# Optimization experiments

Measured on AMD Instinct MI355X. Metric: run time of the kernel, lower is better.

## Reference

```python
import jax, jax.numpy as jnp
import numpy as np


def mha(x, mask, wq, bq, wk, bk, wv, bv, wo, bo, n_heads):
    # Flaubert/XLM MultiHeadAttention (eval mode, dropout = identity).
    bs, qlen, dim = x.shape
    dph = dim // n_heads

    def split_heads(t):  # (bs, qlen, dim) -> (bs, n_heads, qlen, dph)
        return t.reshape(bs, qlen, n_heads, dph).transpose(0, 2, 1, 3)

    q = split_heads(x @ wq + bq) / jnp.sqrt(jnp.asarray(dph, x.dtype))
    k = split_heads(x @ wk + bk)
    v = split_heads(x @ wv + bv)

    scores = jnp.einsum('bhqd,bhkd->bhqk', q, k)  # (bs, h, qlen, klen)
    neg = jnp.finfo(scores.dtype).min
    scores = jnp.where((mask == 0)[:, None, None, :], neg, scores)
    weights = jax.nn.softmax(scores, axis=-1)
    ctx = jnp.einsum('bhqk,bhkd->bhqd', weights, v)
    ctx = ctx.transpose(0, 2, 1, 3).reshape(bs, qlen, dim)
    return ctx @ wo + bo


def setup_inputs() -> dict:
    key = jax.random.key(0)
    ks = jax.random.split(key, 20)
    bs, slen = 4, 1024
    d0, d1 = 192, 66
    std = 0.02
    inp = {
        'x': jax.random.normal(ks[0], (bs, slen, d0), jnp.float32),
        'y': jax.random.normal(ks[1], (bs, slen, d1), jnp.float32),
        'mask0': jax.random.randint(ks[2], (bs, slen), 0, 2, jnp.int32),
        'mask1': jax.random.randint(ks[3], (bs, slen), 0, 2, jnp.int32),
    }
    names0 = ['q0', 'k0', 'v0', 'o0']
    names1 = ['q1', 'k1', 'v1', 'o1']
    for i, n in enumerate(names0):
        inp[n + '_w'] = jax.random.normal(ks[4 + i], (d0, d0), jnp.float32) * std
        inp[n + '_b'] = jnp.zeros((d0,), jnp.float32)
    for i, n in enumerate(names1):
        inp[n + '_w'] = jax.random.normal(ks[8 + i], (d1, d1), jnp.float32) * std
        inp[n + '_b'] = jnp.zeros((d1,), jnp.float32)
    return inp


def reference(x, y, mask0, mask1,
              q0_w, q0_b, k0_w, k0_b, v0_w, v0_b, o0_w, o0_b,
              q1_w, q1_b, k1_w, k1_b, v1_w, v1_b, o1_w, o1_b):
    out0 = mha(x, mask0, q0_w, q0_b, k0_w, k0_b, v0_w, v0_b, o0_w, o0_b, n_heads=16)
    out1 = mha(y, mask1, q1_w, q1_b, k1_w, k1_b, v1_w, v1_b, o1_w, o1_b, n_heads=11)
    return (out0, out1)
```

## Files before the change

### kernel.cpp

```cpp
#include <hip/hip_runtime.h>
#include <math.h>


#define BS 4
#define SLEN 1024

#define Q0_OFF 0
#define C0_OFF 786432
#define Q1_OFF 1572864
#define C1_OFF 1843200
#define K0H_OFF 2113536
#define V0T_OFF 2506752
#define K1H_OFF 2899968
#define V1T_OFF 3080192
#define CNT_OFF 3223552

#define OUT0_SIZE 786432

#if __has_builtin(__builtin_amdgcn_exp2f)
#define EXP2(x) __builtin_amdgcn_exp2f(x)
#else
#define EXP2(x) __expf((x) * 0.69314718056f)
#endif

typedef _Float16 f16x2 __attribute__((ext_vector_type(2)));
typedef _Float16 f16x4 __attribute__((ext_vector_type(4)));
typedef _Float16 f16x8 __attribute__((ext_vector_type(8)));
typedef float f32x4 __attribute__((ext_vector_type(4)));

__device__ __forceinline__ void mfma_chunk(const _Float16* sA, const _Float16* sWT,
                                           int wv, int lane, f32x4 acc[4])
{
  const int col = lane & 15, grp = lane >> 4;
#pragma unroll
  for (int ks = 0; ks < 2; ++ks) {
    const f16x8 bf = *(const f16x8*)(sWT + (wv * 16 + col) * 72 + ks * 32 + grp * 8);
#pragma unroll
    for (int mt = 0; mt < 4; ++mt) {
      const f16x8 af = *(const f16x8*)(sA + (mt * 16 + col) * 72 + ks * 32 + grp * 8);
      acc[mt] = __builtin_amdgcn_mfma_f32_16x16x32_f16(af, bf, acc[mt], 0, 0, 0);
    }
  }
}

__device__ __forceinline__ void mfma_chunk_split(
    const _Float16* sAh, const _Float16* sAl,
    const _Float16* sWTh, const _Float16* sWTl,
    int wv, int lane, f32x4 acc[4])
{
  const int col = lane & 15, grp = lane >> 4;
#pragma unroll
  for (int ks = 0; ks < 2; ++ks) {
    const int boff = (wv * 16 + col) * 72 + ks * 32 + grp * 8;
    const f16x8 bh = *(const f16x8*)(sWTh + boff);
    const f16x8 bl = *(const f16x8*)(sWTl + boff);
#pragma unroll
    for (int mt = 0; mt < 4; ++mt) {
      const int aoff = (mt * 16 + col) * 72 + ks * 32 + grp * 8;
      const f16x8 ah = *(const f16x8*)(sAh + aoff);
      const f16x8 al = *(const f16x8*)(sAl + aoff);
      acc[mt] = __builtin_amdgcn_mfma_f32_16x16x32_f16(ah, bh, acc[mt], 0, 0, 0);
      acc[mt] = __builtin_amdgcn_mfma_f32_16x16x32_f16(ah, bl, acc[mt], 0, 0, 0);
      acc[mt] = __builtin_amdgcn_mfma_f32_16x16x32_f16(al, bh, acc[mt], 0, 0, 0);
    }
  }
}

template <int DIM, int H, int DPH, int NT, int NCH, int KST>
__device__ void qkv_impl(int bid, const float* __restrict__ X,
                         const int* __restrict__ mask,
                         const float* __restrict__ qw, const float* __restrict__ qb,
                         const float* __restrict__ kw, const float* __restrict__ kb,
                         const float* __restrict__ vw, const float* __restrict__ vb,
                         float* __restrict__ qo, _Float16* __restrict__ kh,
                         _Float16* __restrict__ vth, int* __restrict__ cnt_out,
                         char* smem)
{
  const int mt64 = bid & 63;
  const int rest = bid >> 6;
  const int mat = rest / NT;
  const int nt = rest % NT;
  const int row0 = mt64 * 64, col0 = nt * 64;

  const float* W = (mat == 0) ? qw : (mat == 1) ? kw : vw;
  const float* B = (mat == 0) ? qb : (mat == 1) ? kb : vb;
  const float scale = (mat == 0) ? (1.44269504089f / sqrtf((float)DPH)) : 1.0f;

  _Float16* sA = (_Float16*)smem;
  _Float16* sWT = sA + 64 * 72;
  int* sSP = (int*)(smem + 2 * 64 * 72 * 2);

  const int tid = threadIdx.x;
  const int wv = tid >> 6, lane = tid & 63;

  float2 rA[8], rW[8];
  auto qprefetch = [&](int c) {
    const int kc = c * 64;
#pragma unroll
    for (int t = 0; t < 8; ++t) {
      const int idx = tid + t * 256;
      {
        const int m = idx >> 5, k = (idx & 31) * 2;
        rA[t] = (kc + k < DIM)
                    ? *(const float2*)(X + (size_t)(row0 + m) * DIM + kc + k)
                    : make_float2(0.f, 0.f);
      }
      {
        const int k = idx >> 5, n = (idx & 31) * 2;
        rW[t] = (kc + k < DIM && col0 + n < DIM)
                    ? *(const float2*)(W + (size_t)(kc + k) * DIM + col0 + n)
                    : make_float2(0.f, 0.f);
      }
    }
  };
  auto qcommit = [&]() {
#pragma unroll
    for (int t = 0; t < 8; ++t) {
      const int idx = tid + t * 256;
      {
        const int m = idx >> 5, k = (idx & 31) * 2;
        *(f16x2*)(sA + m * 72 + k) = (f16x2){(_Float16)rA[t].x, (_Float16)rA[t].y};
      }
      {
        const int k = idx >> 5, n = (idx & 31) * 2;
        sWT[n * 72 + k] = (_Float16)rW[t].x;
        sWT[(n + 1) * 72 + k] = (_Float16)rW[t].y;
      }
    }
  };

  qprefetch(0);

  if (mat != 0) {
    int* sS = (int*)smem;
    const int b = row0 >> 10;
    const int* m = mask + (b << 10);
    int mv[4], s4 = 0;
#pragma unroll
    for (int i = 0; i < 4; ++i) { mv[i] = m[tid * 4 + i] ? 1 : 0; s4 += mv[i]; }
    sS[tid] = s4;
    __syncthreads();
    for (int off = 1; off < 256; off <<= 1) {
      const int v = sS[tid];
      const int add = (tid >= off) ? sS[tid - off] : 0;
      __syncthreads();
      sS[tid] = v + add;
      __syncthreads();
    }
    const int tot = sS[255];
    int u = tid ? sS[tid - 1] : 0;
    const int s0 = row0 & 1023;
#pragma unroll
    for (int i = 0; i < 4; ++i) {
      const int s = tid * 4 + i;
      const int sp = mv[i] ? u : tot + (s - u);
      u += mv[i];
      const unsigned rel = (unsigned)(s - s0);
      if (rel < 64u) sSP[rel] = sp;
    }
    if (mat == 1 && nt == 0 && s0 == 0 && tid == 0) cnt_out[b] = tot;
    __syncthreads();
  }

  f32x4 acc[4] = {{0.f,0.f,0.f,0.f},{0.f,0.f,0.f,0.f},{0.f,0.f,0.f,0.f},{0.f,0.f,0.f,0.f}};

  for (int c = 0; c < NCH; ++c) {
    __syncthreads();
    qcommit();
    __syncthreads();
    if (c + 1 < NCH) qprefetch(c + 1);
    mfma_chunk(sA, sWT, wv, lane, acc);
  }

  const int col = lane & 15, grp = lane >> 4;
  const int cidx = col0 + wv * 16 + col;
  if (cidx < DIM) {
    const float bias = B[cidx];
    const int h = cidx / DPH, d = cidx % DPH;
#pragma unroll
    for (int mt = 0; mt < 4; ++mt) {
#pragma unroll
      for (int r = 0; r < 4; ++r) {
        const int m = row0 + mt * 16 + grp * 4 + r;
        const int b = m >> 10, s = m & 1023;
        const float v = acc[mt][r] + bias;
        const int bh = b * H + h;
        if (mat == 0) {
          qo[(size_t)((bh << 10) + s) * DPH + d] = v * scale;
        } else {
          const int sp = sSP[mt * 16 + grp * 4 + r];
          if (mat == 1)
            kh[(size_t)((bh << 10) + sp) * KST + d] = (_Float16)v;
          else
            vth[((size_t)(bh * DPH + d) << 10) + sp] = (_Float16)v;
        }
      }
    }
  }
}

__global__ __launch_bounds__(256) void qkv_kernel(
    const float* __restrict__ x, const float* __restrict__ y,
    const int* __restrict__ mask0, const int* __restrict__ mask1,
    const float* __restrict__ q0w, const float* __restrict__ q0b,
    const float* __restrict__ k0w, const float* __restrict__ k0b,
    const float* __restrict__ v0w, const float* __restrict__ v0b,
    const float* __restrict__ q1w, const float* __restrict__ q1b,
    const float* __restrict__ k1w, const float* __restrict__ k1b,
    const float* __restrict__ v1w, const float* __restrict__ v1b,
    float* __restrict__ ws)
{
  extern __shared__ char smem[];
  _Float16* hws = (_Float16*)ws;
  int* cnts = (int*)(ws + CNT_OFF);
  const int bid = blockIdx.x;
  if (bid < 576)
    qkv_impl<192, 16, 12, 3, 3, 12>(bid, x, mask0, q0w, q0b, k0w, k0b, v0w, v0b,
                                    ws + Q0_OFF, hws + 2 * (size_t)K0H_OFF,
                                    hws + 2 * (size_t)V0T_OFF, cnts, smem);
  else
    qkv_impl<66, 11, 6, 2, 2, 8>(bid - 576, y, mask1, q1w, q1b, k1w, k1b, v1w, v1b,
                                 ws + Q1_OFF, hws + 2 * (size_t)K1H_OFF,
                                 hws + 2 * (size_t)V1T_OFF, cnts + 4, smem);
}

template <int H, int DPH, int SKP>
__device__ void attn_impl(int bid, const float* __restrict__ qg,
                          const _Float16* __restrict__ kh,
                          const _Float16* __restrict__ vth,
                          const int* __restrict__ cnts,
                          float* __restrict__ ctx, char* smem)
{
  constexpr int CH = 128;
  constexpr int KBUF = CH * SKP + 32;
  constexpr int VST = 136;

  _Float16* sK = (_Float16*)smem;
  _Float16* sVT = sK + 2 * KBUF;

  const int bh = bid >> 4;
  const int b = bh / H;
  const int h = bh % H;
  const int tid = threadIdx.x;

  const float* qb_ = qg + (size_t)bh * SLEN * DPH;
  const _Float16* kb_ = kh + (size_t)bh * SLEN * SKP;
  const _Float16* vb_ = vth + ((size_t)bh * DPH << 10);
  const int cnt = cnts[b];
  const int nch = (cnt + CH - 1) >> 7;

  if (tid < 64) sK[(tid >> 5) * KBUF + CH * SKP + (tid & 31)] = (_Float16)0.f;

  const int wave = tid >> 6, lane = tid & 63;
  const int col = lane & 15, grp = lane >> 4;
  const int qtile = (bid & 15) * 4 + wave;

  f16x4 aq;
  {
    const int qrow = qtile * 16 + col;
#pragma unroll
    for (int j = 0; j < 4; ++j) {
      const int d = grp * 4 + j;
      aq[j] = (d < DPH) ? (_Float16)qb_[(size_t)qrow * DPH + d] : (_Float16)0.f;
    }
  }

  constexpr int kN = CH * SKP / 8;
  constexpr int vN = DPH * 16;
  const int vd = tid >> 4, vq = tid & 15;
  uint4 pk, pv;
  auto prefetch = [&](int cc) {
    if (tid < kN) pk = ((const uint4*)(kb_ + (size_t)cc * CH * SKP))[tid];
    if (tid < vN) pv = ((const uint4*)(vb_ + ((size_t)vd << 10) + cc * CH))[vq];
  };
  auto commit = [&](int pb) {
    if (tid < kN) ((uint4*)(sK + pb * KBUF))[tid] = pk;
    if (tid < vN) *(uint4*)(sVT + (pb * DPH + vd) * VST + vq * 8) = pv;
  };

  prefetch(0);
  commit(0);
  __syncthreads();

  f32x4 Oacc[2] = {{0.f,0.f,0.f,0.f},{0.f,0.f,0.f,0.f}};
  float lsum = 0.f;
  const int de = (col < DPH) ? col : 0;

#pragma unroll 1
  for (int c = 0; c < nch; ++c) {
    const int p = c & 1;
    if (c + 1 < nch) prefetch(c + 1);

    const _Float16* sKp = sK + p * KBUF;
    const _Float16* sVp = sVT + p * DPH * VST;
    const int keyr = c * CH + grp * 4;

#pragma unroll
    for (int kt = 0; kt < CH / 16; ++kt) {
      const f16x4 kf = *(const f16x4*)(sKp + (kt * 16 + col) * SKP + grp * 4);
      const int k0 = keyr + kt * 16;
      const f32x4 biasv = {(k0 < cnt) ? 0.f : -100.f,
                           (k0 + 1 < cnt) ? 0.f : -100.f,
                           (k0 + 2 < cnt) ? 0.f : -100.f,
                           (k0 + 3 < cnt) ? 0.f : -100.f};
      const f32x4 S = __builtin_amdgcn_mfma_f32_16x16x16f16(kf, aq, biasv,
                                                            0, 0, 0);
      const float e0 = EXP2(S[0]), e1 = EXP2(S[1]);
      const float e2 = EXP2(S[2]), e3 = EXP2(S[3]);
      lsum += (e0 + e1) + (e2 + e3);
      const f16x4 pf = {(_Float16)e0, (_Float16)e1, (_Float16)e2, (_Float16)e3};
      const f16x4 vf = *(const f16x4*)(sVp + de * VST + kt * 16 + grp * 4);
      Oacc[kt & 1] = __builtin_amdgcn_mfma_f32_16x16x16f16(pf, vf, Oacc[kt & 1],
                                                           0, 0, 0);
    }

    if (c + 1 < nch) commit(p ^ 1);
    __syncthreads();
  }

  f32x4 Osum;
#pragma unroll
  for (int r = 0; r < 4; ++r) Osum[r] = Oacc[0][r] + Oacc[1][r];
  float lred = lsum;
  lred += __shfl_xor(lred, 16);
  lred += __shfl_xor(lred, 32);
  float lq[4];
#pragma unroll
  for (int r = 0; r < 4; ++r) lq[r] = __shfl(lred, grp * 4 + r);
  if (col < DPH) {
    const int qrow0 = qtile * 16;
#pragma unroll
    for (int r = 0; r < 4; ++r) {
      const int row = qrow0 + grp * 4 + r;
      ctx[(size_t)(b * SLEN + row) * (H * DPH) + h * DPH + col] = Osum[r] / lq[r];
    }
  }
}

__global__ __launch_bounds__(256) void attn_kernel(float* __restrict__ ws)
{
  extern __shared__ char smem[];
  _Float16* hws = (_Float16*)ws;
  const int* cnts = (const int*)(ws + CNT_OFF);
  const int bid = blockIdx.x;
  if (bid < 1024)
    attn_impl<16, 12, 12>(bid, ws + Q0_OFF, hws + 2 * (size_t)K0H_OFF,
                          hws + 2 * (size_t)V0T_OFF, cnts, ws + C0_OFF, smem);
  else
    attn_impl<11, 6, 8>(bid - 1024, ws + Q1_OFF, hws + 2 * (size_t)K1H_OFF,
                        hws + 2 * (size_t)V1T_OFF, cnts + 4, ws + C1_OFF, smem);
}

template <int DIM, int NCH>
__device__ void oproj_impl(int bid, const float* __restrict__ Cx,
                           const float* __restrict__ ow, const float* __restrict__ ob,
                           float* __restrict__ out, char* smem)
{
  const int mt64 = bid & 63;
  const int nt = bid >> 6;
  const int row0 = mt64 * 64, col0 = nt * 64;

  _Float16* sAh = (_Float16*)smem;
  _Float16* sAl = sAh + 64 * 72;
  _Float16* sWTh = sAl + 64 * 72;
  _Float16* sWTl = sWTh + 64 * 72;

  const int tid = threadIdx.x;
  const int wv = tid >> 6, lane = tid & 63;

  float2 rA[8], rW[8];
  auto oprefetch = [&](int c) {
    const int kc = c * 64;
#pragma unroll
    for (int t = 0; t < 8; ++t) {
      const int idx = tid + t * 256;
      {
        const int m = idx >> 5, k = (idx & 31) * 2;
        rA[t] = (kc + k < DIM)
                    ? *(const float2*)(Cx + (size_t)(row0 + m) * DIM + kc + k)
                    : make_float2(0.f, 0.f);
      }
      {
        const int k = idx >> 5, n = (idx & 31) * 2;
        rW[t] = (kc + k < DIM && col0 + n < DIM)
                    ? *(const float2*)(ow + (size_t)(kc + k) * DIM + col0 + n)
                    : make_float2(0.f, 0.f);
      }
    }
  };
  auto ocommit = [&]() {
#pragma unroll
    for (int t = 0; t < 8; ++t) {
      const int idx = tid + t * 256;
      {
        const int m = idx >> 5, k = (idx & 31) * 2;
        const _Float16 hx = (_Float16)rA[t].x, hy = (_Float16)rA[t].y;
        *(f16x2*)(sAh + m * 72 + k) = (f16x2){hx, hy};
        *(f16x2*)(sAl + m * 72 + k) =
            (f16x2){(_Float16)(rA[t].x - (float)hx), (_Float16)(rA[t].y - (float)hy)};
      }
      {
        const int k = idx >> 5, n = (idx & 31) * 2;
        const _Float16 hx = (_Float16)rW[t].x, hy = (_Float16)rW[t].y;
        sWTh[n * 72 + k] = hx;
        sWTh[(n + 1) * 72 + k] = hy;
        sWTl[n * 72 + k] = (_Float16)(rW[t].x - (float)hx);
        sWTl[(n + 1) * 72 + k] = (_Float16)(rW[t].y - (float)hy);
      }
    }
  };

  oprefetch(0);

  f32x4 acc[4] = {{0.f,0.f,0.f,0.f},{0.f,0.f,0.f,0.f},{0.f,0.f,0.f,0.f},{0.f,0.f,0.f,0.f}};

  for (int c = 0; c < NCH; ++c) {
    __syncthreads();
    ocommit();
    __syncthreads();
    if (c + 1 < NCH) oprefetch(c + 1);
    mfma_chunk_split(sAh, sAl, sWTh, sWTl, wv, lane, acc);
  }

  const int col = lane & 15, grp = lane >> 4;
  const int cidx = col0 + wv * 16 + col;
  if (cidx < DIM) {
    const float bias = ob[cidx];
#pragma unroll
    for (int mt = 0; mt < 4; ++mt) {
#pragma unroll
      for (int r = 0; r < 4; ++r) {
        const int m = row0 + mt * 16 + grp * 4 + r;
        out[(size_t)m * DIM + cidx] = acc[mt][r] + bias;
      }
    }
  }
}

__global__ __launch_bounds__(256) void oproj_kernel(
    const float* __restrict__ o0w, const float* __restrict__ o0b,
    const float* __restrict__ o1w, const float* __restrict__ o1b,
    float* __restrict__ ws, float* __restrict__ out)
{
  extern __shared__ char smem[];
  const int bid = blockIdx.x;
  if (bid < 192)
    oproj_impl<192, 3>(bid, ws + C0_OFF, o0w, o0b, out, smem);
  else
    oproj_impl<66, 2>(bid - 192, ws + C1_OFF, o1w, o1b, out + OUT0_SIZE, smem);
}

extern "C" void kernel_launch(void* const* d_in, const int* in_sizes, int n_in,
                              void* d_out, int out_size, void* d_ws, size_t ws_size,
                              hipStream_t stream)
{
  const float* x = (const float*)d_in[0];
  const float* y = (const float*)d_in[1];
  const int* mask0 = (const int*)d_in[2];
  const int* mask1 = (const int*)d_in[3];
  const float* q0w = (const float*)d_in[4];  const float* q0b = (const float*)d_in[5];
  const float* k0w = (const float*)d_in[6];  const float* k0b = (const float*)d_in[7];
  const float* v0w = (const float*)d_in[8];  const float* v0b = (const float*)d_in[9];
  const float* o0w = (const float*)d_in[10]; const float* o0b = (const float*)d_in[11];
  const float* q1w = (const float*)d_in[12]; const float* q1b = (const float*)d_in[13];
  const float* k1w = (const float*)d_in[14]; const float* k1b = (const float*)d_in[15];
  const float* v1w = (const float*)d_in[16]; const float* v1b = (const float*)d_in[17];
  const float* o1w = (const float*)d_in[18]; const float* o1b = (const float*)d_in[19];

  float* ws = (float*)d_ws;
  float* out = (float*)d_out;

  const int qkv_smem = 2 * 64 * 72 * 2 + 64 * 4;
  const int oproj_smem = 4 * 64 * 72 * 2;
  const int attn_smem = 2 * (128 * 12 + 32) * 2 + 2 * 12 * 136 * 2;

  qkv_kernel<<<960, 256, qkv_smem, stream>>>(x, y, mask0, mask1,
                                             q0w, q0b, k0w, k0b, v0w, v0b,
                                             q1w, q1b, k1w, k1b, v1w, v1b, ws);
  attn_kernel<<<1728, 256, attn_smem, stream>>>(ws);
  oproj_kernel<<<320, 256, oproj_smem, stream>>>(o0w, o0b, o1w, o1b, ws, out);
}
```

Before: 144.4 us.

## Fuse output projection into attention via last-head-done atomic counter

```diff
diff --git a/kernel.cpp b/kernel.cpp
--- a/kernel.cpp
+++ b/kernel.cpp
@@ -14,6 +14,11 @@
 #define K1H_OFF 2899968
 #define V1T_OFF 3080192
 #define CNT_OFF 3223552
+#define GRP_OFF 3223560
+#define WT0H_OFF 3223696
+#define WT0L_OFF 3242128
+#define WT1H_OFF 3260560
+#define WT1L_OFF 3263728
 
 #define OUT0_SIZE 786432
 
@@ -39,29 +44,6 @@
     for (int mt = 0; mt < 4; ++mt) {
       const f16x8 af = *(const f16x8*)(sA + (mt * 16 + col) * 72 + ks * 32 + grp * 8);
       acc[mt] = __builtin_amdgcn_mfma_f32_16x16x32_f16(af, bf, acc[mt], 0, 0, 0);
-    }
-  }
-}
-
-__device__ __forceinline__ void mfma_chunk_split(
-    const _Float16* sAh, const _Float16* sAl,
-    const _Float16* sWTh, const _Float16* sWTl,
-    int wv, int lane, f32x4 acc[4])
-{
-  const int col = lane & 15, grp = lane >> 4;
-#pragma unroll
-  for (int ks = 0; ks < 2; ++ks) {
-    const int boff = (wv * 16 + col) * 72 + ks * 32 + grp * 8;
-    const f16x8 bh = *(const f16x8*)(sWTh + boff);
-    const f16x8 bl = *(const f16x8*)(sWTl + boff);
-#pragma unroll
-    for (int mt = 0; mt < 4; ++mt) {
-      const int aoff = (mt * 16 + col) * 72 + ks * 32 + grp * 8;
-      const f16x8 ah = *(const f16x8*)(sAh + aoff);
-      const f16x8 al = *(const f16x8*)(sAl + aoff);
-      acc[mt] = __builtin_amdgcn_mfma_f32_16x16x32_f16(ah, bh, acc[mt], 0, 0, 0);
-      acc[mt] = __builtin_amdgcn_mfma_f32_16x16x32_f16(ah, bl, acc[mt], 0, 0, 0);
-      acc[mt] = __builtin_amdgcn_mfma_f32_16x16x32_f16(al, bh, acc[mt], 0, 0, 0);
     }
   }
 }
@@ -199,6 +181,34 @@
   }
 }
 
+__device__ void qkv_aux(int aid, const float* __restrict__ o0w,
+                        const float* __restrict__ o1w,
+                        _Float16* __restrict__ wt0h, _Float16* __restrict__ wt0l,
+                        _Float16* __restrict__ wt1h, _Float16* __restrict__ wt1l,
+                        int* __restrict__ grp)
+{
+  const int tid = threadIdx.x;
+  if (aid == 0 && tid < 128) grp[tid] = 0;
+  if (aid < 6) {
+    for (int e = aid * 6144 + tid; e < (aid + 1) * 6144; e += 256) {
+      const int n = e / 192, k = e - n * 192;
+      const float v = o0w[k * 192 + n];
+      const _Float16 h = (_Float16)v;
+      wt0h[n * 192 + k] = h;
+      wt0l[n * 192 + k] = (_Float16)(v - (float)h);
+    }
+  } else {
+    const int a = aid - 6;
+    for (int e = a * 3168 + tid; e < (a + 1) * 3168; e += 256) {
+      const int n = e / 96, k = e - n * 96;
+      const float v = (k < 66) ? o1w[k * 66 + n] : 0.f;
+      const _Float16 h = (_Float16)v;
+      wt1h[n * 96 + k] = h;
+      wt1l[n * 96 + k] = (_Float16)(v - (float)h);
+    }
+  }
+}
+
 __global__ __launch_bounds__(256) void qkv_kernel(
     const float* __restrict__ x, const float* __restrict__ y,
     const int* __restrict__ mask0, const int* __restrict__ mask1,
@@ -208,12 +218,20 @@
     const float* __restrict__ q1w, const float* __restrict__ q1b,
     const float* __restrict__ k1w, const float* __restrict__ k1b,
     const float* __restrict__ v1w, const float* __restrict__ v1b,
+    const float* __restrict__ o0w, const float* __restrict__ o1w,
     float* __restrict__ ws)
 {
   extern __shared__ char smem[];
   _Float16* hws = (_Float16*)ws;
   int* cnts = (int*)(ws + CNT_OFF);
   const int bid = blockIdx.x;
+  if (bid >= 960) {
+    qkv_aux(bid - 960, o0w, o1w,
+            hws + 2 * (size_t)WT0H_OFF, hws + 2 * (size_t)WT0L_OFF,
+            hws + 2 * (size_t)WT1H_OFF, hws + 2 * (size_t)WT1L_OFF,
+            (int*)(ws + GRP_OFF));
+    return;
+  }
   if (bid < 576)
     qkv_impl<192, 16, 12, 3, 3, 12>(bid, x, mask0, q0w, q0b, k0w, k0b, v0w, v0b,
                                     ws + Q0_OFF, hws + 2 * (size_t)K0H_OFF,
@@ -224,12 +242,17 @@
                                  hws + 2 * (size_t)V1T_OFF, cnts + 4, smem);
 }
 
-template <int H, int DPH, int SKP>
+template <int H, int DPH, int SKP, int DIMo, int NT, int NKB, int KP, bool VEC>
 __device__ void attn_impl(int bid, const float* __restrict__ qg,
                           const _Float16* __restrict__ kh,
                           const _Float16* __restrict__ vth,
                           const int* __restrict__ cnts,
-                          float* __restrict__ ctx, char* smem)
+                          float* __restrict__ ctx,
+                          const _Float16* __restrict__ WTh,
+                          const _Float16* __restrict__ WTl,
+                          const float* __restrict__ obias,
+                          float* __restrict__ outp,
+                          int* __restrict__ grp, int gbase, char* smem)
 {
   constexpr int CH = 128;
   constexpr int KBUF = CH * SKP + 32;
@@ -252,7 +275,7 @@
   if (tid < 64) sK[(tid >> 5) * KBUF + CH * SKP + (tid & 31)] = (_Float16)0.f;
 
   const int wave = tid >> 6, lane = tid & 63;
-  const int col = lane & 15, grp = lane >> 4;
+  const int col = lane & 15, grpq = lane >> 4;
   const int qtile = (bid & 15) * 4 + wave;
 
   f16x4 aq;
@@ -260,7 +283,7 @@
     const int qrow = qtile * 16 + col;
 #pragma unroll
     for (int j = 0; j < 4; ++j) {
-      const int d = grp * 4 + j;
+      const int d = grpq * 4 + j;
       aq[j] = (d < DPH) ? (_Float16)qb_[(size_t)qrow * DPH + d] : (_Float16)0.f;
     }
   }
@@ -293,11 +316,11 @@
 
     const _Float16* sKp = sK + p * KBUF;
     const _Float16* sVp = sVT + p * DPH * VST;
-    const int keyr = c * CH + grp * 4;
+    const int keyr = c * CH + grpq * 4;
 
 #pragma unroll
     for (int kt = 0; kt < CH / 16; ++kt) {
-      const f16x4 kf = *(const f16x4*)(sKp + (kt * 16 + col) * SKP + grp * 4);
+      const f16x4 kf = *(const f16x4*)(sKp + (kt * 16 + col) * SKP + grpq * 4);
       const int k0 = keyr + kt * 16;
       const f32x4 biasv = {(k0 < cnt) ? 0.f : -100.f,
                            (k0 + 1 < cnt) ? 0.f : -100.f,
@@ -309,7 +332,7 @@
       const float e2 = EXP2(S[2]), e3 = EXP2(S[3]);
       lsum += (e0 + e1) + (e2 + e3);
       const f16x4 pf = {(_Float16)e0, (_Float16)e1, (_Float16)e2, (_Float16)e3};
-      const f16x4 vf = *(const f16x4*)(sVp + de * VST + kt * 16 + grp * 4);
+      const f16x4 vf = *(const f16x4*)(sVp + de * VST + kt * 16 + grpq * 4);
       Oacc[kt & 1] = __builtin_amdgcn_mfma_f32_16x16x16f16(pf, vf, Oacc[kt & 1],
                                                            0, 0, 0);
     }
@@ -326,128 +349,104 @@
   lred += __shfl_xor(lred, 32);
   float lq[4];
 #pragma unroll
-  for (int r = 0; r < 4; ++r) lq[r] = __shfl(lred, grp * 4 + r);
+  for (int r = 0; r < 4; ++r) lq[r] = __shfl(lred, grpq * 4 + r);
   if (col < DPH) {
     const int qrow0 = qtile * 16;
 #pragma unroll
     for (int r = 0; r < 4; ++r) {
-      const int row = qrow0 + grp * 4 + r;
+      const int row = qrow0 + grpq * 4 + r;
       ctx[(size_t)(b * SLEN + row) * (H * DPH) + h * DPH + col] = Osum[r] / lq[r];
     }
   }
-}
-
-__global__ __launch_bounds__(256) void attn_kernel(float* __restrict__ ws)
+
+  __threadfence();
+  __syncthreads();
+  int* flag = (int*)smem;
+  if (tid == 0) {
+    const int g = gbase + b * 16 + (bid & 15);
+    flag[0] = (atomicAdd(&grp[g], 1) == H - 1) ? 1 : 0;
+  }
+  __syncthreads();
+  if (!flag[0]) return;
+  __threadfence();
+
+  const int strip = bid & 15;
+  const float* Crow = ctx + (size_t)(b * SLEN + strip * 64) * DIMo;
+  float* Orow = outp + (size_t)(b * SLEN + strip * 64) * DIMo;
+
+#pragma unroll 1
+  for (int nt = 0; nt < NT; ++nt) {
+    const int cidx = nt * 64 + wave * 16 + col;
+    f32x4 oacc[4] = {{0.f,0.f,0.f,0.f},{0.f,0.f,0.f,0.f},
+                     {0.f,0.f,0.f,0.f},{0.f,0.f,0.f,0.f}};
+#pragma unroll
+    for (int kb = 0; kb < NKB; ++kb) {
+      const int k0 = kb * 32 + grpq * 8;
+      f16x8 bhf = {}, blf = {};
+      if (cidx < DIMo) {
+        bhf = *(const f16x8*)(WTh + (size_t)cidx * KP + k0);
+        blf = *(const f16x8*)(WTl + (size_t)cidx * KP + k0);
+      }
+#pragma unroll
+      for (int mt = 0; mt < 4; ++mt) {
+        const int row_a = mt * 16 + col;
+        f16x8 ah, al;
+        if (VEC) {
+          const float* ap = Crow + (size_t)row_a * DIMo + k0;
+          const f32x4 v0 = *(const f32x4*)(ap);
+          const f32x4 v1 = *(const f32x4*)(ap + 4);
+#pragma unroll
+          for (int j = 0; j < 4; ++j) {
+            const _Float16 h0 = (_Float16)v0[j];
+            ah[j] = h0; al[j] = (_Float16)(v0[j] - (float)h0);
+            const _Float16 h1 = (_Float16)v1[j];
+            ah[4 + j] = h1; al[4 + j] = (_Float16)(v1[j] - (float)h1);
+          }
+        } else {
+#pragma unroll
+          for (int j = 0; j < 8; ++j) {
+            const int k = k0 + j;
+            const float v = (k < DIMo) ? Crow[(size_t)row_a * DIMo + k] : 0.f;
+            const _Float16 hh = (_Float16)v;
+            ah[j] = hh; al[j] = (_Float16)(v - (float)hh);
+          }
+        }
+        oacc[mt] = __builtin_amdgcn_mfma_f32_16x16x32_f16(ah, bhf, oacc[mt], 0, 0, 0);
+        oacc[mt] = __builtin_amdgcn_mfma_f32_16x16x32_f16(ah, blf, oacc[mt], 0, 0, 0);
+        oacc[mt] = __builtin_amdgcn_mfma_f32_16x16x32_f16(al, bhf, oacc[mt], 0, 0, 0);
+      }
+    }
+    if (cidx < DIMo) {
+      const float bias = obias[cidx];
+#pragma unroll
+      for (int mt = 0; mt < 4; ++mt)
+#pragma unroll
+        for (int r = 0; r < 4; ++r)
+          Orow[(size_t)(mt * 16 + grpq * 4 + r) * DIMo + cidx] = oacc[mt][r] + bias;
+    }
+  }
+}
+
+__global__ __launch_bounds__(256) void attn_kernel(
+    float* __restrict__ ws, float* __restrict__ out,
+    const float* __restrict__ o0b, const float* __restrict__ o1b)
 {
   extern __shared__ char smem[];
   _Float16* hws = (_Float16*)ws;
   const int* cnts = (const int*)(ws + CNT_OFF);
+  int* grp = (int*)(ws + GRP_OFF);
   const int bid = blockIdx.x;
   if (bid < 1024)
-    attn_impl<16, 12, 12>(bid, ws + Q0_OFF, hws + 2 * (size_t)K0H_OFF,
-                          hws + 2 * (size_t)V0T_OFF, cnts, ws + C0_OFF, smem);
+    attn_impl<16, 12, 12, 192, 3, 6, 192, true>(
+        bid, ws + Q0_OFF, hws + 2 * (size_t)K0H_OFF, hws + 2 * (size_t)V0T_OFF,
+        cnts, ws + C0_OFF, hws + 2 * (size_t)WT0H_OFF, hws + 2 * (size_t)WT0L_OFF,
+        o0b, out, grp, 0, smem);
   else
-    attn_impl<11, 6, 8>(bid - 1024, ws + Q1_OFF, hws + 2 * (size_t)K1H_OFF,
-                        hws + 2 * (size_t)V1T_OFF, cnts + 4, ws + C1_OFF, smem);
-}
-
-template <int DIM, int NCH>
-__device__ void oproj_impl(int bid, const float* __restrict__ Cx,
-                           const float* __restrict__ ow, const float* __restrict__ ob,
-                           float* __restrict__ out, char* smem)
-{
-  const int mt64 = bid & 63;
-  const int nt = bid >> 6;
-  const int row0 = mt64 * 64, col0 = nt * 64;
-
-  _Float16* sAh = (_Float16*)smem;
-  _Float16* sAl = sAh + 64 * 72;
-  _Float16* sWTh = sAl + 64 * 72;
-  _Float16* sWTl = sWTh + 64 * 72;
-
-  const int tid = threadIdx.x;
-  const int wv = tid >> 6, lane = tid & 63;
-
-  float2 rA[8], rW[8];
-  auto oprefetch = [&](int c) {
-    const int kc = c * 64;
-#pragma unroll
-    for (int t = 0; t < 8; ++t) {
-      const int idx = tid + t * 256;
-      {
-        const int m = idx >> 5, k = (idx & 31) * 2;
-        rA[t] = (kc + k < DIM)
-                    ? *(const float2*)(Cx + (size_t)(row0 + m) * DIM + kc + k)
-                    : make_float2(0.f, 0.f);
-      }
-      {
-        const int k = idx >> 5, n = (idx & 31) * 2;
-        rW[t] = (kc + k < DIM && col0 + n < DIM)
-                    ? *(const float2*)(ow + (size_t)(kc + k) * DIM + col0 + n)
-                    : make_float2(0.f, 0.f);
-      }
-    }
-  };
-  auto ocommit = [&]() {
-#pragma unroll
-    for (int t = 0; t < 8; ++t) {
-      const int idx = tid + t * 256;
-      {
-        const int m = idx >> 5, k = (idx & 31) * 2;
-        const _Float16 hx = (_Float16)rA[t].x, hy = (_Float16)rA[t].y;
-        *(f16x2*)(sAh + m * 72 + k) = (f16x2){hx, hy};
-        *(f16x2*)(sAl + m * 72 + k) =
-            (f16x2){(_Float16)(rA[t].x - (float)hx), (_Float16)(rA[t].y - (float)hy)};
-      }
-      {
-        const int k = idx >> 5, n = (idx & 31) * 2;
-        const _Float16 hx = (_Float16)rW[t].x, hy = (_Float16)rW[t].y;
-        sWTh[n * 72 + k] = hx;
-        sWTh[(n + 1) * 72 + k] = hy;
-        sWTl[n * 72 + k] = (_Float16)(rW[t].x - (float)hx);
-        sWTl[(n + 1) * 72 + k] = (_Float16)(rW[t].y - (float)hy);
-      }
-    }
-  };
-
-  oprefetch(0);
-
-  f32x4 acc[4] = {{0.f,0.f,0.f,0.f},{0.f,0.f,0.f,0.f},{0.f,0.f,0.f,0.f},{0.f,0.f,0.f,0.f}};
-
-  for (int c = 0; c < NCH; ++c) {
-    __syncthreads();
-    ocommit();
-    __syncthreads();
-    if (c + 1 < NCH) oprefetch(c + 1);
-    mfma_chunk_split(sAh, sAl, sWTh, sWTl, wv, lane, acc);
-  }
-
-  const int col = lane & 15, grp = lane >> 4;
-  const int cidx = col0 + wv * 16 + col;
-  if (cidx < DIM) {
-    const float bias = ob[cidx];
-#pragma unroll
-    for (int mt = 0; mt < 4; ++mt) {
-#pragma unroll
-      for (int r = 0; r < 4; ++r) {
-        const int m = row0 + mt * 16 + grp * 4 + r;
-        out[(size_t)m * DIM + cidx] = acc[mt][r] + bias;
-      }
-    }
-  }
-}
-
-__global__ __launch_bounds__(256) void oproj_kernel(
-    const float* __restrict__ o0w, const float* __restrict__ o0b,
-    const float* __restrict__ o1w, const float* __restrict__ o1b,
-    float* __restrict__ ws, float* __restrict__ out)
-{
-  extern __shared__ char smem[];
-  const int bid = blockIdx.x;
-  if (bid < 192)
-    oproj_impl<192, 3>(bid, ws + C0_OFF, o0w, o0b, out, smem);
-  else
-    oproj_impl<66, 2>(bid - 192, ws + C1_OFF, o1w, o1b, out + OUT0_SIZE, smem);
+    attn_impl<11, 6, 8, 66, 2, 3, 96, false>(
+        bid - 1024, ws + Q1_OFF, hws + 2 * (size_t)K1H_OFF,
+        hws + 2 * (size_t)V1T_OFF, cnts + 4, ws + C1_OFF,
+        hws + 2 * (size_t)WT1H_OFF, hws + 2 * (size_t)WT1L_OFF,
+        o1b, out + OUT0_SIZE, grp, 64, smem);
 }
 
 extern "C" void kernel_launch(void* const* d_in, const int* in_sizes, int n_in,
@@ -471,12 +470,11 @@
   float* out = (float*)d_out;
 
   const int qkv_smem = 2 * 64 * 72 * 2 + 64 * 4;
-  const int oproj_smem = 4 * 64 * 72 * 2;
   const int attn_smem = 2 * (128 * 12 + 32) * 2 + 2 * 12 * 136 * 2;
 
-  qkv_kernel<<<960, 256, qkv_smem, stream>>>(x, y, mask0, mask1,
+  qkv_kernel<<<968, 256, qkv_smem, stream>>>(x, y, mask0, mask1,
                                              q0w, q0b, k0w, k0b, v0w, v0b,
-                                             q1w, q1b, k1w, k1b, v1w, v1b, ws);
-  attn_kernel<<<1728, 256, attn_smem, stream>>>(ws);
-  oproj_kernel<<<320, 256, oproj_smem, stream>>>(o0w, o0b, o1w, o1b, ws, out);
-}
+                                             q1w, q1b, k1w, k1b, v1w, v1b,
+                                             o0w, o1w, ws);
+  attn_kernel<<<1728, 256, attn_smem, stream>>>(ws, out, o0b, o1b);
+}
```

Result: slower. 323.2 us (+123.7%).

## Process two query tiles per wave in attention and halve oproj row tiles

Applied to the files above, without the earlier changes.

```diff
diff --git a/kernel.cpp b/kernel.cpp
--- a/kernel.cpp
+++ b/kernel.cpp
@@ -43,10 +43,11 @@
   }
 }
 
+template <int MT>
 __device__ __forceinline__ void mfma_chunk_split(
     const _Float16* sAh, const _Float16* sAl,
     const _Float16* sWTh, const _Float16* sWTl,
-    int wv, int lane, f32x4 acc[4])
+    int wv, int lane, f32x4 acc[MT])
 {
   const int col = lane & 15, grp = lane >> 4;
 #pragma unroll
@@ -55,7 +56,7 @@
     const f16x8 bh = *(const f16x8*)(sWTh + boff);
     const f16x8 bl = *(const f16x8*)(sWTl + boff);
 #pragma unroll
-    for (int mt = 0; mt < 4; ++mt) {
+    for (int mt = 0; mt < MT; ++mt) {
       const int aoff = (mt * 16 + col) * 72 + ks * 32 + grp * 8;
       const f16x8 ah = *(const f16x8*)(sAh + aoff);
       const f16x8 al = *(const f16x8*)(sAl + aoff);
@@ -238,7 +239,7 @@
   _Float16* sK = (_Float16*)smem;
   _Float16* sVT = sK + 2 * KBUF;
 
-  const int bh = bid >> 4;
+  const int bh = bid >> 3;
   const int b = bh / H;
   const int h = bh % H;
   const int tid = threadIdx.x;
@@ -253,15 +254,17 @@
 
   const int wave = tid >> 6, lane = tid & 63;
   const int col = lane & 15, grp = lane >> 4;
-  const int qtile = (bid & 15) * 4 + wave;
-
-  f16x4 aq;
-  {
-    const int qrow = qtile * 16 + col;
+  const int strip = bid & 7;
+  const int qt[2] = {strip * 8 + wave, strip * 8 + 4 + wave};
+
+  f16x4 aq[2];
+#pragma unroll
+  for (int i = 0; i < 2; ++i) {
+    const int qrow = qt[i] * 16 + col;
 #pragma unroll
     for (int j = 0; j < 4; ++j) {
       const int d = grp * 4 + j;
-      aq[j] = (d < DPH) ? (_Float16)qb_[(size_t)qrow * DPH + d] : (_Float16)0.f;
+      aq[i][j] = (d < DPH) ? (_Float16)qb_[(size_t)qrow * DPH + d] : (_Float16)0.f;
     }
   }
 
@@ -282,8 +285,9 @@
   commit(0);
   __syncthreads();
 
-  f32x4 Oacc[2] = {{0.f,0.f,0.f,0.f},{0.f,0.f,0.f,0.f}};
-  float lsum = 0.f;
+  f32x4 Oacc[2][2] = {{{0.f,0.f,0.f,0.f},{0.f,0.f,0.f,0.f}},
+                      {{0.f,0.f,0.f,0.f},{0.f,0.f,0.f,0.f}}};
+  float lsum[2] = {0.f, 0.f};
   const int de = (col < DPH) ? col : 0;
 
 #pragma unroll 1
@@ -303,36 +307,49 @@
                            (k0 + 1 < cnt) ? 0.f : -100.f,
                            (k0 + 2 < cnt) ? 0.f : -100.f,
                            (k0 + 3 < cnt) ? 0.f : -100.f};
-      const f32x4 S = __builtin_amdgcn_mfma_f32_16x16x16f16(kf, aq, biasv,
-                                                            0, 0, 0);
-      const float e0 = EXP2(S[0]), e1 = EXP2(S[1]);
-      const float e2 = EXP2(S[2]), e3 = EXP2(S[3]);
-      lsum += (e0 + e1) + (e2 + e3);
-      const f16x4 pf = {(_Float16)e0, (_Float16)e1, (_Float16)e2, (_Float16)e3};
+      const f32x4 S0 = __builtin_amdgcn_mfma_f32_16x16x16f16(kf, aq[0], biasv,
+                                                             0, 0, 0);
+      const f32x4 S1 = __builtin_amdgcn_mfma_f32_16x16x16f16(kf, aq[1], biasv,
+                                                             0, 0, 0);
       const f16x4 vf = *(const f16x4*)(sVp + de * VST + kt * 16 + grp * 4);
-      Oacc[kt & 1] = __builtin_amdgcn_mfma_f32_16x16x16f16(pf, vf, Oacc[kt & 1],
-                                                           0, 0, 0);
+      const float a0 = EXP2(S0[0]), a1 = EXP2(S0[1]);
+      const float a2 = EXP2(S0[2]), a3 = EXP2(S0[3]);
+      lsum[0] += (a0 + a1) + (a2 + a3);
+      const f16x4 pf0 = {(_Float16)a0, (_Float16)a1, (_Float16)a2, (_Float16)a3};
+      Oacc[0][kt & 1] = __builtin_amdgcn_mfma_f32_16x16x16f16(pf0, vf,
+                                                              Oacc[0][kt & 1],
+                                                              0, 0, 0);
+      const float b0 = EXP2(S1[0]), b1 = EXP2(S1[1]);
+      const float b2 = EXP2(S1[2]), b3 = EXP2(S1[3]);
+      lsum[1] += (b0 + b1) + (b2 + b3);
+      const f16x4 pf1 = {(_Float16)b0, (_Float16)b1, (_Float16)b2, (_Float16)b3};
+      Oacc[1][kt & 1] = __builtin_amdgcn_mfma_f32_16x16x16f16(pf1, vf,
+                                                              Oacc[1][kt & 1],
+                                                              0, 0, 0);
     }
 
     if (c + 1 < nch) commit(p ^ 1);
     __syncthreads();
   }
 
-  f32x4 Osum;
-#pragma unroll
-  for (int r = 0; r < 4; ++r) Osum[r] = Oacc[0][r] + Oacc[1][r];
-  float lred = lsum;
-  lred += __shfl_xor(lred, 16);
-  lred += __shfl_xor(lred, 32);
-  float lq[4];
-#pragma unroll
-  for (int r = 0; r < 4; ++r) lq[r] = __shfl(lred, grp * 4 + r);
-  if (col < DPH) {
-    const int qrow0 = qtile * 16;
-#pragma unroll
-    for (int r = 0; r < 4; ++r) {
-      const int row = qrow0 + grp * 4 + r;
-      ctx[(size_t)(b * SLEN + row) * (H * DPH) + h * DPH + col] = Osum[r] / lq[r];
+#pragma unroll
+  for (int i = 0; i < 2; ++i) {
+    f32x4 Osum;
+#pragma unroll
+    for (int r = 0; r < 4; ++r) Osum[r] = Oacc[i][0][r] + Oacc[i][1][r];
+    float lred = lsum[i];
+    lred += __shfl_xor(lred, 16);
+    lred += __shfl_xor(lred, 32);
+    float lq[4];
+#pragma unroll
+    for (int r = 0; r < 4; ++r) lq[r] = __shfl(lred, grp * 4 + r);
+    if (col < DPH) {
+      const int qrow0 = qt[i] * 16;
+#pragma unroll
+      for (int r = 0; r < 4; ++r) {
+        const int row = qrow0 + grp * 4 + r;
+        ctx[(size_t)(b * SLEN + row) * (H * DPH) + h * DPH + col] = Osum[r] / lq[r];
+      }
     }
   }
 }
@@ -343,11 +360,11 @@
   _Float16* hws = (_Float16*)ws;
   const int* cnts = (const int*)(ws + CNT_OFF);
   const int bid = blockIdx.x;
-  if (bid < 1024)
+  if (bid < 512)
     attn_impl<16, 12, 12>(bid, ws + Q0_OFF, hws + 2 * (size_t)K0H_OFF,
                           hws + 2 * (size_t)V0T_OFF, cnts, ws + C0_OFF, smem);
   else
-    attn_impl<11, 6, 8>(bid - 1024, ws + Q1_OFF, hws + 2 * (size_t)K1H_OFF,
+    attn_impl<11, 6, 8>(bid - 512, ws + Q1_OFF, hws + 2 * (size_t)K1H_OFF,
                         hws + 2 * (size_t)V1T_OFF, cnts + 4, ws + C1_OFF, smem);
 }
 
@@ -356,70 +373,70 @@
                            const float* __restrict__ ow, const float* __restrict__ ob,
                            float* __restrict__ out, char* smem)
 {
-  const int mt64 = bid & 63;
-  const int nt = bid >> 6;
-  const int row0 = mt64 * 64, col0 = nt * 64;
+  const int mt128 = bid & 127;
+  const int nt = bid >> 7;
+  const int row0 = mt128 * 32, col0 = nt * 64;
 
   _Float16* sAh = (_Float16*)smem;
-  _Float16* sAl = sAh + 64 * 72;
-  _Float16* sWTh = sAl + 64 * 72;
+  _Float16* sAl = sAh + 32 * 72;
+  _Float16* sWTh = sAl + 32 * 72;
   _Float16* sWTl = sWTh + 64 * 72;
 
   const int tid = threadIdx.x;
   const int wv = tid >> 6, lane = tid & 63;
 
-  float2 rA[8], rW[8];
+  float2 rA[4], rW[8];
   auto oprefetch = [&](int c) {
     const int kc = c * 64;
 #pragma unroll
+    for (int t = 0; t < 4; ++t) {
+      const int idx = tid + t * 256;
+      const int m = idx >> 5, k = (idx & 31) * 2;
+      rA[t] = (kc + k < DIM)
+                  ? *(const float2*)(Cx + (size_t)(row0 + m) * DIM + kc + k)
+                  : make_float2(0.f, 0.f);
+    }
+#pragma unroll
     for (int t = 0; t < 8; ++t) {
       const int idx = tid + t * 256;
-      {
-        const int m = idx >> 5, k = (idx & 31) * 2;
-        rA[t] = (kc + k < DIM)
-                    ? *(const float2*)(Cx + (size_t)(row0 + m) * DIM + kc + k)
-                    : make_float2(0.f, 0.f);
-      }
-      {
-        const int k = idx >> 5, n = (idx & 31) * 2;
-        rW[t] = (kc + k < DIM && col0 + n < DIM)
-                    ? *(const float2*)(ow + (size_t)(kc + k) * DIM + col0 + n)
-                    : make_float2(0.f, 0.f);
-      }
+      const int k = idx >> 5, n = (idx & 31) * 2;
+      rW[t] = (kc + k < DIM && col0 + n < DIM)
+                  ? *(const float2*)(ow + (size_t)(kc + k) * DIM + col0 + n)
+                  : make_float2(0.f, 0.f);
     }
   };
   auto ocommit = [&]() {
 #pragma unroll
+    for (int t = 0; t < 4; ++t) {
+      const int idx = tid + t * 256;
+      const int m = idx >> 5, k = (idx & 31) * 2;
+      const _Float16 hx = (_Float16)rA[t].x, hy = (_Float16)rA[t].y;
+      *(f16x2*)(sAh + m * 72 + k) = (f16x2){hx, hy};
+      *(f16x2*)(sAl + m * 72 + k) =
+          (f16x2){(_Float16)(rA[t].x - (float)hx), (_Float16)(rA[t].y - (float)hy)};
+    }
+#pragma unroll
     for (int t = 0; t < 8; ++t) {
       const int idx = tid + t * 256;
-      {
-        const int m = idx >> 5, k = (idx & 31) * 2;
-        const _Float16 hx = (_Float16)rA[t].x, hy = (_Float16)rA[t].y;
-        *(f16x2*)(sAh + m * 72 + k) = (f16x2){hx, hy};
-        *(f16x2*)(sAl + m * 72 + k) =
-            (f16x2){(_Float16)(rA[t].x - (float)hx), (_Float16)(rA[t].y - (float)hy)};
-      }
-      {
-        const int k = idx >> 5, n = (idx & 31) * 2;
-        const _Float16 hx = (_Float16)rW[t].x, hy = (_Float16)rW[t].y;
-        sWTh[n * 72 + k] = hx;
-        sWTh[(n + 1) * 72 + k] = hy;
-        sWTl[n * 72 + k] = (_Float16)(rW[t].x - (float)hx);
-        sWTl[(n + 1) * 72 + k] = (_Float16)(rW[t].y - (float)hy);
-      }
+      const int k = idx >> 5, n = (idx & 31) * 2;
+      const _Float16 hx = (_Float16)rW[t].x, hy = (_Float16)rW[t].y;
+      sWTh[n * 72 + k] = hx;
+      sWTh[(n + 1) * 72 + k] = hy;
+      sWTl[n * 72 + k] = (_Float16)(rW[t].x - (float)hx);
+      sWTl[(n + 1) * 72 + k] = (_Float16)(rW[t].y - (float)hy);
     }
   };
 
   oprefetch(0);
 
-  f32x4 acc[4] = {{0.f,0.f,0.f,0.f},{0.f,0.f,0.f,0.f},{0.f,0.f,0.f,0.f},{0.f,0.f,0.f,0.f}};
+  f32x4 acc[2] = {{0.f,0.f,0.f,0.f},{0.f,0.f,0.f,0.f}};
 
   for (int c = 0; c < NCH; ++c) {
     __syncthreads();
     ocommit();
     __syncthreads();
     if (c + 1 < NCH) oprefetch(c + 1);
-    mfma_chunk_split(sAh, sAl, sWTh, sWTl, wv, lane, acc);
+    mfma_chunk_split<2>(sAh, sAl, sWTh, sWTl, wv, lane, acc);
   }
 
   const int col = lane & 15, grp = lane >> 4;
@@ -427,7 +444,7 @@
   if (cidx < DIM) {
     const float bias = ob[cidx];
 #pragma unroll
-    for (int mt = 0; mt < 4; ++mt) {
+    for (int mt = 0; mt < 2; ++mt) {
 #pragma unroll
       for (int r = 0; r < 4; ++r) {
         const int m = row0 + mt * 16 + grp * 4 + r;
@@ -444,10 +461,10 @@
 {
   extern __shared__ char smem[];
   const int bid = blockIdx.x;
-  if (bid < 192)
+  if (bid < 384)
     oproj_impl<192, 3>(bid, ws + C0_OFF, o0w, o0b, out, smem);
   else
-    oproj_impl<66, 2>(bid - 192, ws + C1_OFF, o1w, o1b, out + OUT0_SIZE, smem);
+    oproj_impl<66, 2>(bid - 384, ws + C1_OFF, o1w, o1b, out + OUT0_SIZE, smem);
 }
 
 extern "C" void kernel_launch(void* const* d_in, const int* in_sizes, int n_in,
@@ -471,12 +488,12 @@
   float* out = (float*)d_out;
 
   const int qkv_smem = 2 * 64 * 72 * 2 + 64 * 4;
-  const int oproj_smem = 4 * 64 * 72 * 2;
+  const int oproj_smem = (2 * 32 * 72 + 2 * 64 * 72) * 2;
   const int attn_smem = 2 * (128 * 12 + 32) * 2 + 2 * 12 * 136 * 2;
 
   qkv_kernel<<<960, 256, qkv_smem, stream>>>(x, y, mask0, mask1,
                                              q0w, q0b, k0w, k0b, v0w, v0b,
                                              q1w, q1b, k1w, k1b, v1w, v1b, ws);
-  attn_kernel<<<1728, 256, attn_smem, stream>>>(ws);
-  oproj_kernel<<<320, 256, oproj_smem, stream>>>(o0w, o0b, o1w, o1b, ws, out);
-}
+  attn_kernel<<<864, 256, attn_smem, stream>>>(ws);
+  oproj_kernel<<<640, 256, oproj_smem, stream>>>(o0w, o0b, o1w, o1b, ws, out);
+}
```

New measurement: 143.6 us. Within noise of the previous version (-0.6%).
